# Optimization experiments

Hardware: AMD Instinct MI355X
Metric: run time of the kernel (lower is better)

Reference implementation:

```python
import jax, jax.numpy as jnp
import numpy as np

D = 256      # word_embd_size
V = 32000    # vocab_size_w
B, T, J = 32, 512, 128


def _gru_dir(x, wih, whh, bih, bhh):
    # x: (B, T, D); torch GRU cell convention
    def step(h, xt):
        gi = xt @ wih.T + bih            # (B, 3D)
        gh = h @ whh.T + bhh
        i_r, i_z, i_n = jnp.split(gi, 3, axis=-1)
        h_r, h_z, h_n = jnp.split(gh, 3, axis=-1)
        r = jax.nn.sigmoid(i_r + h_r)
        z = jax.nn.sigmoid(i_z + h_z)
        n = jnp.tanh(i_n + r * h_n)
        h_new = (1.0 - z) * n + z * h
        return h_new, h_new
    h0 = jnp.zeros((x.shape[0], D), dtype=x.dtype)
    _, ys = jax.lax.scan(step, h0, jnp.swapaxes(x, 0, 1))
    return jnp.swapaxes(ys, 0, 1)         # (B, T, D)


def _bigru(x, wih_f, whh_f, bih_f, bhh_f, wih_b, whh_b, bih_b, bhh_b):
    fwd = _gru_dir(x, wih_f, whh_f, bih_f, bhh_f)
    bwd = jnp.flip(_gru_dir(jnp.flip(x, 1), wih_b, whh_b, bih_b, bhh_b), 1)
    return jnp.concatenate([fwd, bwd], axis=-1)   # (B, T, 2D)


def _cmnt_sim(ctx, cmnt_e, action, w2):
    # Fused form of: S = W2_ha(cat(ctx_ex * cmnt_ex, action_ex)) over (B,T,J,2D+1)
    # S[b,t,j] = sum_d ctx[b,t,d]*cmnt[b,j,d]*w2[d] + action[b,t]*w2[2D]
    S = jnp.einsum('btd,bjd->btj', ctx * w2[:2 * D], cmnt_e)
    S = S + action.astype(ctx.dtype)[:, :, None] * w2[2 * D]
    b = jax.nn.softmax(jnp.max(S, axis=2), axis=-1)   # (B, T)
    return jnp.einsum('bt,btj->bj', b, S)             # (B, J)


def setup_inputs() -> dict:
    key = jax.random.key(0)
    ks = jax.random.split(key, 20)
    s = 1.0 / np.sqrt(D)
    u = lambda k, shape: jax.random.uniform(k, shape, minval=-s, maxval=s, dtype=jnp.float32)
    return {
        'cmnt': jax.random.randint(ks[0], (B, J), 0, V),
        'src_token': jax.random.randint(ks[1], (B, T), 0, V),
        'tgt_token': jax.random.randint(ks[2], (B, T), 0, V),
        'src_action': jax.random.randint(ks[3], (B, T), 0, 2),
        'tgt_action': jax.random.randint(ks[4], (B, T), 0, 2),
        'emb': jax.random.normal(ks[5], (V, D), dtype=jnp.float32) * 0.02,
        'wih_f': u(ks[6], (3 * D, D)), 'whh_f': u(ks[7], (3 * D, D)),
        'bih_f': u(ks[8], (3 * D,)),  'bhh_f': u(ks[9], (3 * D,)),
        'wih_b': u(ks[10], (3 * D, D)), 'whh_b': u(ks[11], (3 * D, D)),
        'bih_b': u(ks[12], (3 * D,)),  'bhh_b': u(ks[13], (3 * D,)),
        'w2': u(ks[14], (2 * D + 1,)),
        'rank_w': u(ks[15], (2 * J, 1)),
        'rank_b': u(ks[16], (1,)),
    }


def reference(cmnt, src_token, tgt_token, src_action, tgt_action, emb,
              wih_f, whh_f, bih_f, bhh_f, wih_b, whh_b, bih_b, bhh_b,
              w2, rank_w, rank_b):
    gru = lambda x: _bigru(x, wih_f, whh_f, bih_f, bhh_f, wih_b, whh_b, bih_b, bhh_b)
    e_src = gru(emb[src_token])    # (B, T, 2D)
    e_tgt = gru(emb[tgt_token])    # (B, T, 2D)
    e_cmnt = gru(emb[cmnt])        # (B, J, 2D)
    S_src = _cmnt_sim(e_src, e_cmnt, src_action, w2)
    S_tgt = _cmnt_sim(e_tgt, e_cmnt, tgt_action, w2)
    S_diff = jnp.concatenate([S_src, S_tgt], axis=1)   # (B, 2J)
    result = S_diff @ rank_w + rank_b                   # (B, 1)
    return result, S_diff
```

## Files before the change

kernel.cpp:

```cpp
#include <hip/hip_runtime.h>
#include <math.h>

#define DD   256
#define TTT  512
#define JJJ  128
#define BBB  32
#define NC   1536
#define ROWS_ALL 36864

typedef _Float16 v2h __attribute__((ext_vector_type(2)));
typedef _Float16 v4h __attribute__((ext_vector_type(4)));
typedef _Float16 v8h __attribute__((ext_vector_type(8)));
typedef short short8 __attribute__((ext_vector_type(8)));
typedef float f32x4 __attribute__((ext_vector_type(4)));

#if __has_builtin(__builtin_amdgcn_fdot2)
#define FDOT2(a, b, c) __builtin_amdgcn_fdot2((a), (b), (c), false)
#else
#define FDOT2(a, b, c) ((float)(a)[0] * (float)(b)[0] + ((float)(a)[1] * (float)(b)[1] + (c)))
#endif

__device__ __forceinline__ short f2bf(float f) {
    unsigned u = __float_as_uint(f);
    unsigned r = (u + 0x7FFFu + ((u >> 16) & 1u)) >> 16;
    return (short)r;
}

__global__ __launch_bounds__(256) void prep_kernel(
    const int* __restrict__ cmnt, const int* __restrict__ src_tok, const int* __restrict__ tgt_tok,
    const float* __restrict__ wih_f, const float* __restrict__ wih_b,
    const float* __restrict__ whh_f, const float* __restrict__ whh_b,
    const float* __restrict__ bih_f, const float* __restrict__ bih_b,
    const float* __restrict__ bhh_f, const float* __restrict__ bhh_b,
    const float* __restrict__ w2,
    int* __restrict__ tok_all, float* __restrict__ whhT,
    float* __restrict__ bihc, float* __restrict__ bhhc, short* __restrict__ Bt,
    _Float16* __restrict__ w2h)
{
    const int idx = blockIdx.x * blockDim.x + threadIdx.x;
    const int stride = gridDim.x * blockDim.x;
    for (int i = idx; i < ROWS_ALL; i += stride)
        tok_all[i] = (i < 16384) ? src_tok[i] : (i < 32768) ? tgt_tok[i - 16384] : cmnt[i - 32768];
    for (int i = idx; i < 256 * NC; i += stride) {
        const int k = i / NC, c = i % NC;
        whhT[i] = (c < 768) ? whh_f[(size_t)c * 256 + k] : whh_b[(size_t)(c - 768) * 256 + k];
    }
    for (int i = idx; i < 393216; i += stride)
        Bt[i] = f2bf(i < 196608 ? wih_f[i] : wih_b[i - 196608]);
    for (int i = idx; i < NC; i += stride) {
        bihc[i] = (i < 768) ? bih_f[i] : bih_b[i - 768];
        bhhc[i] = (i < 768) ? bhh_f[i] : bhh_b[i - 768];
    }
    for (int i = idx; i < 512; i += stride)
        w2h[i] = (_Float16)w2[i];
}

__global__ __launch_bounds__(256) void gatherA_kernel(
    const int* __restrict__ tok, int row_start, int nrows,
    const float* __restrict__ emb, short* __restrict__ A)
{
    const int idx = blockIdx.x * blockDim.x + threadIdx.x;
    const int stride = gridDim.x * blockDim.x;
    const int ngroups = nrows * 64;
    for (int g = idx; g < ngroups; g += stride) {
        const int i = g >> 6;
        const int kq = (g & 63) << 2;
        const float4 v = *(const float4*)(emb + (size_t)tok[row_start + i] * 256 + kq);
        short4 s;
        s.x = f2bf(v.x); s.y = f2bf(v.y); s.z = f2bf(v.z); s.w = f2bf(v.w);
        *(short4*)(A + (size_t)i * 256 + kq) = s;
    }
}

#define LP 40
__global__ __launch_bounds__(256) void gi_mfma(
    const short* __restrict__ A, const short* __restrict__ Bt,
    const float* __restrict__ bihc, _Float16* __restrict__ gi)
{
    __shared__ __align__(16) short As[128 * LP];
    __shared__ __align__(16) short Bs[128 * LP];
    const int tid = threadIdx.x;
    const int wave = tid >> 6, lane = tid & 63;
    const int quad = lane >> 4, l16 = lane & 15;
    const int m0 = blockIdx.x * 128, n0 = blockIdx.y * 128;
    const int wm = (wave & 1) * 64, wn = (wave >> 1) * 64;

    const int sr = tid >> 2;
    const int sk = (tid & 3) * 8;
    const short* ga0 = A  + (size_t)(m0 + sr) * 256 + sk;
    const short* ga1 = A  + (size_t)(m0 + sr + 64) * 256 + sk;
    const short* gb0 = Bt + (size_t)(n0 + sr) * 256 + sk;
    const short* gb1 = Bt + (size_t)(n0 + sr + 64) * 256 + sk;

    f32x4 acc[4][4];
    #pragma unroll
    for (int i = 0; i < 4; ++i)
        #pragma unroll
        for (int j = 0; j < 4; ++j) acc[i][j] = (f32x4){0.f, 0.f, 0.f, 0.f};

    for (int k0 = 0; k0 < 256; k0 += 32) {
        const short8 a0 = *(const short8*)(ga0 + k0);
        const short8 a1 = *(const short8*)(ga1 + k0);
        const short8 b0 = *(const short8*)(gb0 + k0);
        const short8 b1 = *(const short8*)(gb1 + k0);
        __syncthreads();
        *(short8*)&As[sr * LP + sk] = a0;
        *(short8*)&As[(sr + 64) * LP + sk] = a1;
        *(short8*)&Bs[sr * LP + sk] = b0;
        *(short8*)&Bs[(sr + 64) * LP + sk] = b1;
        __syncthreads();
        short8 af[4], bf[4];
        #pragma unroll
        for (int i = 0; i < 4; ++i)
            af[i] = *(const short8*)&As[(wm + i * 16 + l16) * LP + quad * 8];
        #pragma unroll
        for (int j = 0; j < 4; ++j)
            bf[j] = *(const short8*)&Bs[(wn + j * 16 + l16) * LP + quad * 8];
        #pragma unroll
        for (int i = 0; i < 4; ++i)
            #pragma unroll
            for (int j = 0; j < 4; ++j)
                acc[i][j] = __builtin_amdgcn_mfma_f32_16x16x32_bf16(af[i], bf[j], acc[i][j], 0, 0, 0);
    }

    #pragma unroll
    for (int j = 0; j < 4; ++j) {
        const int col = n0 + wn + j * 16 + l16;
        const float bias = bihc[col];
        #pragma unroll
        for (int i = 0; i < 4; ++i) {
            const int r0 = m0 + wm + i * 16 + quad * 4;
            #pragma unroll
            for (int reg = 0; reg < 4; ++reg)
                gi[(size_t)(r0 + reg) * NC + col] = (_Float16)(acc[i][j][reg] + bias);
        }
    }
}

__global__ __launch_bounds__(512, 2) void gru_kernel(
    const _Float16* __restrict__ gi0, const _Float16* __restrict__ gi1, const _Float16* __restrict__ gi2,
    const float* __restrict__ whhT, const float* __restrict__ bhhc,
    _Float16* __restrict__ e_src, _Float16* __restrict__ e_tgt, _Float16* __restrict__ e_cmnt,
    int chain_base)
{
    const int chain = chain_base + (int)(blockIdx.x >> 5);
    const int b = (int)(blockIdx.x & 31);
    const int seq = chain >> 1, dir = chain & 1;
    const int Tlen = (seq == 2) ? JJJ : TTT;
    const _Float16* gi = (seq == 0) ? gi0 : (seq == 1) ? gi1 : gi2;
    _Float16* e = (seq == 0) ? e_src : (seq == 1) ? e_tgt : e_cmnt;

    const int tid = threadIdx.x;
    const int j = tid & 255;
    const int q = tid >> 8;
    const int cb = dir * 768;

    __shared__ __align__(16) v2h h2s[128];
    __shared__ float parts[3][256];

    v2h wr2[64], wz2[64], wn2[64];
    {
        const float* wb = whhT + (size_t)(q * 128) * NC + cb + j;
        #pragma unroll
        for (int p = 0; p < 64; ++p) {
            v2h a, bzv, c;
            a[0]   = (_Float16)wb[0];        a[1]   = (_Float16)wb[NC];
            bzv[0] = (_Float16)wb[256];      bzv[1] = (_Float16)wb[NC + 256];
            c[0]   = (_Float16)wb[512];      c[1]   = (_Float16)wb[NC + 512];
            wr2[p] = a; wz2[p] = bzv; wn2[p] = c;
            wb += 2 * NC;
        }
    }
    const float br  = bhhc[cb + j];
    const float bzb = bhhc[cb + 256 + j];
    const float bnb = bhhc[cb + 512 + j];

    float hprev = 0.f;
    if (q == 0 && (j & 1) == 0) {
        v2h z0; z0[0] = (_Float16)0.f; z0[1] = (_Float16)0.f;
        h2s[j >> 1] = z0;
    }
    __syncthreads();

    const int t0i = dir ? (Tlen - 1) : 0;
    const long tstep = dir ? -1 : 1;
    const _Float16* girow = gi + (size_t)(b * Tlen + t0i) * NC + cb;
    _Float16* eptr = e + (size_t)(b * Tlen + t0i) * 512 + (dir << 8) + j;
    const long gstep = tstep * NC;
    const long estep = tstep * 512;

    _Float16* pptr = eptr;
    float pval = 0.f;

    for (int s = 0; s < Tlen; ++s) {
        float gr_ = 0.f, gz_ = 0.f, gn_ = 0.f;
        if (q == 0) {
            if (s > 0) *pptr = (_Float16)pval;
            gr_ = (float)girow[j];
            gz_ = (float)girow[256 + j];
            gn_ = (float)girow[512 + j];
        }

        float ar = 0.f, az = 0.f, an = 0.f;
        const v2h* hbase = &h2s[q * 64];
        #pragma unroll
        for (int c = 0; c < 16; ++c) {
            union { float4 f; v2h h[4]; } U;
            U.f = *(const float4*)&hbase[c * 4];
            #pragma unroll
            for (int p = 0; p < 4; ++p) {
                ar = FDOT2(wr2[c * 4 + p], U.h[p], ar);
                az = FDOT2(wz2[c * 4 + p], U.h[p], az);
                an = FDOT2(wn2[c * 4 + p], U.h[p], an);
            }
        }
        if (q == 1) { parts[0][j] = ar; parts[1][j] = az; parts[2][j] = an; }
        __syncthreads();

        if (q == 0) {
            const float sr = ar + parts[0][j] + br;
            const float sz = az + parts[1][j] + bzb;
            const float sn = an + parts[2][j] + bnb;
            const float r = 1.f / (1.f + __expf(-(gr_ + sr)));
            const float z = 1.f / (1.f + __expf(-(gz_ + sz)));
            const float xa = gn_ + r * sn;
            const float texp = __expf(2.f * xa);
            const float n = 1.f - 2.f / (texp + 1.f);
            const float hnew = (1.f - z) * n + z * hprev;
            hprev = hnew;
            pptr = eptr; pval = hnew;
            const float hnb = __shfl_xor(hnew, 1);
            if ((j & 1) == 0) {
                v2h hv; hv[0] = (_Float16)hnew; hv[1] = (_Float16)hnb;
                h2s[j >> 1] = hv;
            }
        }
        girow += gstep;
        eptr += estep;
        __syncthreads();
    }
    if (q == 0) *pptr = (_Float16)pval;
}

__global__ __launch_bounds__(256) void sim_mfma(
    const _Float16* __restrict__ e_src, const _Float16* __restrict__ e_tgt,
    const _Float16* __restrict__ e_cmnt, const _Float16* __restrict__ w2h,
    const float* __restrict__ w2,
    const int* __restrict__ src_action, const int* __restrict__ tgt_action,
    float* __restrict__ S, float* __restrict__ rowmaxP)
{
    const int sb = (int)blockIdx.z;
    const int seq = sb >> 5, b = sb & 31;
    const int t0 = blockIdx.x * 128;
    const _Float16* ctx = ((seq == 0) ? e_src : e_tgt) + (size_t)b * 512 * 512;
    const _Float16* ec = e_cmnt + (size_t)b * 128 * 512;
    const int* act = (seq == 0) ? src_action : tgt_action;

    __shared__ __align__(16) _Float16 As[128 * LP];
    __shared__ __align__(16) _Float16 Bs[128 * LP];
    const int tid = threadIdx.x;
    const int wave = tid >> 6, lane = tid & 63;
    const int quad = lane >> 4, l16 = lane & 15;
    const int wm = (wave & 1) * 64, wn = (wave >> 1) * 64;
    const int sr = tid >> 2;
    const int sk = (tid & 3) * 8;

    const _Float16* ga0 = ctx + (size_t)(t0 + sr) * 512 + sk;
    const _Float16* ga1 = ctx + (size_t)(t0 + sr + 64) * 512 + sk;
    const _Float16* gb0 = ec + (size_t)sr * 512 + sk;
    const _Float16* gb1 = ec + (size_t)(sr + 64) * 512 + sk;

    f32x4 acc[4][4];
    #pragma unroll
    for (int i = 0; i < 4; ++i)
        #pragma unroll
        for (int j = 0; j < 4; ++j) acc[i][j] = (f32x4){0.f, 0.f, 0.f, 0.f};

    for (int k0 = 0; k0 < 512; k0 += 32) {
        v8h a0 = *(const v8h*)(ga0 + k0);
        v8h a1 = *(const v8h*)(ga1 + k0);
        const v8h b0 = *(const v8h*)(gb0 + k0);
        const v8h b1 = *(const v8h*)(gb1 + k0);
        const v8h w8 = *(const v8h*)(w2h + k0 + sk);
        a0 = a0 * w8;
        a1 = a1 * w8;
        __syncthreads();
        *(v8h*)&As[sr * LP + sk] = a0;
        *(v8h*)&As[(sr + 64) * LP + sk] = a1;
        *(v8h*)&Bs[sr * LP + sk] = b0;
        *(v8h*)&Bs[(sr + 64) * LP + sk] = b1;
        __syncthreads();
        v8h af[4], bf[4];
        #pragma unroll
        for (int i = 0; i < 4; ++i)
            af[i] = *(const v8h*)&As[(wm + i * 16 + l16) * LP + quad * 8];
        #pragma unroll
        for (int j = 0; j < 4; ++j)
            bf[j] = *(const v8h*)&Bs[(wn + j * 16 + l16) * LP + quad * 8];
        #pragma unroll
        for (int i = 0; i < 4; ++i)
            #pragma unroll
            for (int j = 0; j < 4; ++j)
                acc[i][j] = __builtin_amdgcn_mfma_f32_16x16x32_f16(af[i], bf[j], acc[i][j], 0, 0, 0);
    }

    const float w2a = w2[512];
    #pragma unroll
    for (int i = 0; i < 4; ++i) {
        #pragma unroll
        for (int reg = 0; reg < 4; ++reg) {
            const int t = t0 + wm + i * 16 + quad * 4 + reg;
            const float aterm = (float)act[b * 512 + t] * w2a;
            float m = -1e30f;
            #pragma unroll
            for (int j = 0; j < 4; ++j) {
                const float v = acc[i][j][reg] + aterm;
                S[((size_t)(sb * 512 + t)) * 128 + wn + j * 16 + l16] = v;
                m = fmaxf(m, v);
            }
            m = fmaxf(m, __shfl_xor(m, 1));
            m = fmaxf(m, __shfl_xor(m, 2));
            m = fmaxf(m, __shfl_xor(m, 4));
            m = fmaxf(m, __shfl_xor(m, 8));
            if (l16 == 0)
                rowmaxP[(size_t)(wave >> 1) * 32768 + sb * 512 + t] = m;
        }
    }
}

__global__ __launch_bounds__(256) void softmax_kernel(const float* __restrict__ rowmaxP, float* __restrict__ bw)
{
    const int base = blockIdx.x * 512;
    const int tid = threadIdx.x;
    __shared__ float red[256];
    const float v0 = fmaxf(rowmaxP[base + tid], rowmaxP[32768 + base + tid]);
    const float v1 = fmaxf(rowmaxP[base + 256 + tid], rowmaxP[32768 + base + 256 + tid]);
    red[tid] = fmaxf(v0, v1);
    __syncthreads();
    for (int off = 128; off > 0; off >>= 1) {
        if (tid < off) red[tid] = fmaxf(red[tid], red[tid + off]);
        __syncthreads();
    }
    const float M = red[0];
    __syncthreads();
    const float e0 = __expf(v0 - M), e1 = __expf(v1 - M);
    red[tid] = e0 + e1;
    __syncthreads();
    for (int off = 128; off > 0; off >>= 1) {
        if (tid < off) red[tid] += red[tid + off];
        __syncthreads();
    }
    const float inv = 1.f / red[0];
    bw[base + tid] = e0 * inv;
    bw[base + 256 + tid] = e1 * inv;
}

__global__ __launch_bounds__(256) void weighted_kernel(
    const float* __restrict__ S, const float* __restrict__ bw, float* __restrict__ outSP)
{
    const int sb = blockIdx.x;
    const int ch = blockIdx.y;
    const int tid = threadIdx.x;
    const int j = tid & 127, half = tid >> 7;
    const float* Sb = S + (size_t)sb * 512 * 128;
    const float* w = bw + sb * 512;
    const int tb = ch * 64 + half * 32;
    float acc = 0.f;
    for (int t = tb; t < tb + 32; ++t)
        acc = fmaf(w[t], Sb[(size_t)t * 128 + j], acc);
    __shared__ float red[256];
    red[tid] = acc;
    __syncthreads();
    if (half == 0) outSP[(size_t)ch * 8192 + sb * 128 + j] = red[j] + red[128 + j];
}

__global__ __launch_bounds__(256) void final_kernel(
    const float* __restrict__ outSP, const float* __restrict__ rank_w,
    const float* __restrict__ rank_b, float* __restrict__ out)
{
    __shared__ float sArr[8192];
    const int tid = threadIdx.x;
    for (int q = tid; q < 8192; q += 256) {
        float s = 0.f;
        #pragma unroll
        for (int c = 0; c < 8; ++c) s += outSP[(size_t)c * 8192 + q];
        sArr[q] = s;
    }
    __syncthreads();
    for (int q = tid; q < 8192; q += 256) {
        const int b = q >> 8, c = q & 255;
        out[32 + q] = (c < 128) ? sArr[b * 128 + c] : sArr[4096 + b * 128 + (c - 128)];
    }
    if (tid < 32) {
        float acc = rank_b[0];
        for (int c = 0; c < 128; ++c) acc = fmaf(sArr[tid * 128 + c], rank_w[c], acc);
        for (int c = 0; c < 128; ++c) acc = fmaf(sArr[4096 + tid * 128 + c], rank_w[128 + c], acc);
        out[tid] = acc;
    }
}

extern "C" void kernel_launch(void* const* d_in, const int* in_sizes, int n_in,
                              void* d_out, int out_size, void* d_ws, size_t ws_size,
                              hipStream_t stream)
{
    const int* cmnt       = (const int*)d_in[0];
    const int* src_token  = (const int*)d_in[1];
    const int* tgt_token  = (const int*)d_in[2];
    const int* src_action = (const int*)d_in[3];
    const int* tgt_action = (const int*)d_in[4];
    const float* emb    = (const float*)d_in[5];
    const float* wih_f  = (const float*)d_in[6];
    const float* whh_f  = (const float*)d_in[7];
    const float* bih_f  = (const float*)d_in[8];
    const float* bhh_f  = (const float*)d_in[9];
    const float* wih_b  = (const float*)d_in[10];
    const float* whh_b  = (const float*)d_in[11];
    const float* bih_b  = (const float*)d_in[12];
    const float* bhh_b  = (const float*)d_in[13];
    const float* w2     = (const float*)d_in[14];
    const float* rank_w = (const float*)d_in[15];
    const float* rank_b = (const float*)d_in[16];
    float* out = (float*)d_out;

    float* ws = (float*)d_ws;
    size_t off = 0;
    int*   tok_all = (int*)(ws + off); off += 36864;
    short* Bt_bf16 = (short*)(ws + off); off += 196608;
    float* whhT   = ws + off; off += 393216;
    float* bihc   = ws + off; off += 1536;
    float* bhhc   = ws + off; off += 1536;
    _Float16* w2h = (_Float16*)(ws + off); off += 256;
    float* rowmaxP = ws + off; off += 65536;
    float* bw     = ws + off; off += 32768;
    float* outSP  = ws + off; off += 65536;
    _Float16* e_src  = (_Float16*)(ws + off); off += 4194304;
    _Float16* e_tgt  = (_Float16*)(ws + off); off += 4194304;
    _Float16* e_cmnt = (_Float16*)(ws + off); off += 1048576;
    float* S      = ws + off; off += 4194304;
    _Float16* gih = (_Float16*)(ws + off);
    const size_t avail = ws_size / 4 - off;
    const bool planP = avail >= 28311552ULL;

    hipLaunchKernelGGL(prep_kernel, dim3(512), dim3(256), 0, stream,
        cmnt, src_token, tgt_token, wih_f, wih_b, whh_f, whh_b,
        bih_f, bih_b, bhh_f, bhh_b, w2, tok_all, whhT, bihc, bhhc, Bt_bf16, w2h);

    if (planP) {
        short* A = (short*)e_src;
        hipLaunchKernelGGL(gatherA_kernel, dim3(4096), dim3(256), 0, stream,
            tok_all, 0, 36864, emb, A);
        hipLaunchKernelGGL(gi_mfma, dim3(288, 12), dim3(256), 0, stream,
            A, Bt_bf16, bihc, gih);
        hipLaunchKernelGGL(gru_kernel, dim3(192), dim3(512), 0, stream,
            gih, gih + (size_t)16384 * NC, gih + (size_t)32768 * NC,
            whhT, bhhc, e_src, e_tgt, e_cmnt, 0);
    } else {
        short* A = (short*)S;
        const int starts[3] = {0, 16384, 32768};
        const int nrows[3]  = {16384, 16384, 4096};
        for (int sq = 0; sq < 3; ++sq) {
            hipLaunchKernelGGL(gatherA_kernel, dim3(4096), dim3(256), 0, stream,
                tok_all, starts[sq], nrows[sq], emb, A);
            hipLaunchKernelGGL(gi_mfma, dim3(nrows[sq] / 128, 12), dim3(256), 0, stream,
                A, Bt_bf16, bihc, gih);
            hipLaunchKernelGGL(gru_kernel, dim3(64), dim3(512), 0, stream,
                gih, gih, gih, whhT, bhhc, e_src, e_tgt, e_cmnt, 2 * sq);
        }
    }

    hipLaunchKernelGGL(sim_mfma, dim3(4, 1, 64), dim3(256), 0, stream,
        e_src, e_tgt, e_cmnt, w2h, w2, src_action, tgt_action, S, rowmaxP);
    hipLaunchKernelGGL(softmax_kernel, dim3(64), dim3(256), 0, stream, rowmaxP, bw);
    hipLaunchKernelGGL(weighted_kernel, dim3(64, 8), dim3(256), 0, stream, S, bw, outSP);
    hipLaunchKernelGGL(final_kernel, dim3(1), dim3(256), 0, stream, outSP, rank_w, rank_b, out);
}
```

Baseline: 844.8 us.

## Batch GRU recurrence over 16 sequences per block using MFMA

The GRU recurrence kernel is restructured so that each block handles 16 batch rows of one chain and runs the h·Whh^T product with f16 MFMA instructions, keeping Whh fragments in registers. Previously each block ran a single batch element with scalar fdot2 and a split-K reduction through shared memory. The input-gate GEMM now writes its output in a swizzled layout matched to the MFMA lane mapping and folds the r/z hidden biases into it. The low-memory fallback plan is removed. The grid shrinks from 192 blocks to 12, so only 12 CUs work through the long sequential chain. Each step now does larger MFMA work per block, which risks poor overall occupancy.

```diff
diff --git a/kernel.cpp b/kernel.cpp
--- a/kernel.cpp
+++ b/kernel.cpp
@@ -13,12 +13,6 @@
 typedef _Float16 v8h __attribute__((ext_vector_type(8)));
 typedef short short8 __attribute__((ext_vector_type(8)));
 typedef float f32x4 __attribute__((ext_vector_type(4)));
-
-#if __has_builtin(__builtin_amdgcn_fdot2)
-#define FDOT2(a, b, c) __builtin_amdgcn_fdot2((a), (b), (c), false)
-#else
-#define FDOT2(a, b, c) ((float)(a)[0] * (float)(b)[0] + ((float)(a)[1] * (float)(b)[1] + (c)))
-#endif
 
 __device__ __forceinline__ short f2bf(float f) {
     unsigned u = __float_as_uint(f);
@@ -33,7 +27,7 @@
     const float* __restrict__ bih_f, const float* __restrict__ bih_b,
     const float* __restrict__ bhh_f, const float* __restrict__ bhh_b,
     const float* __restrict__ w2,
-    int* __restrict__ tok_all, float* __restrict__ whhT,
+    int* __restrict__ tok_all, _Float16* __restrict__ wh16,
     float* __restrict__ bihc, float* __restrict__ bhhc, short* __restrict__ Bt,
     _Float16* __restrict__ w2h)
 {
@@ -41,10 +35,8 @@
     const int stride = gridDim.x * blockDim.x;
     for (int i = idx; i < ROWS_ALL; i += stride)
         tok_all[i] = (i < 16384) ? src_tok[i] : (i < 32768) ? tgt_tok[i - 16384] : cmnt[i - 32768];
-    for (int i = idx; i < 256 * NC; i += stride) {
-        const int k = i / NC, c = i % NC;
-        whhT[i] = (c < 768) ? whh_f[(size_t)c * 256 + k] : whh_b[(size_t)(c - 768) * 256 + k];
-    }
+    for (int i = idx; i < 393216; i += stride)
+        wh16[i] = (_Float16)(i < 196608 ? whh_f[i] : whh_b[i - 196608]);
     for (int i = idx; i < 393216; i += stride)
         Bt[i] = f2bf(i < 196608 ? wih_f[i] : wih_b[i - 196608]);
     for (int i = idx; i < NC; i += stride) {
@@ -56,7 +48,7 @@
 }
 
 __global__ __launch_bounds__(256) void gatherA_kernel(
-    const int* __restrict__ tok, int row_start, int nrows,
+    const int* __restrict__ tok, int nrows,
     const float* __restrict__ emb, short* __restrict__ A)
 {
     const int idx = blockIdx.x * blockDim.x + threadIdx.x;
@@ -65,7 +57,7 @@
     for (int g = idx; g < ngroups; g += stride) {
         const int i = g >> 6;
         const int kq = (g & 63) << 2;
-        const float4 v = *(const float4*)(emb + (size_t)tok[row_start + i] * 256 + kq);
+        const float4 v = *(const float4*)(emb + (size_t)tok[i] * 256 + kq);
         short4 s;
         s.x = f2bf(v.x); s.y = f2bf(v.y); s.z = f2bf(v.z); s.w = f2bf(v.w);
         *(short4*)(A + (size_t)i * 256 + kq) = s;
@@ -75,7 +67,8 @@
 #define LP 40
 __global__ __launch_bounds__(256) void gi_mfma(
     const short* __restrict__ A, const short* __restrict__ Bt,
-    const float* __restrict__ bihc, _Float16* __restrict__ gi)
+    const float* __restrict__ bihc, const float* __restrict__ bhhc,
+    _Float16* __restrict__ gi_swz)
 {
     __shared__ __align__(16) short As[128 * LP];
     __shared__ __align__(16) short Bs[128 * LP];
@@ -123,123 +116,151 @@
                 acc[i][j] = __builtin_amdgcn_mfma_f32_16x16x32_bf16(af[i], bf[j], acc[i][j], 0, 0, 0);
     }
 
-    #pragma unroll
-    for (int j = 0; j < 4; ++j) {
-        const int col = n0 + wn + j * 16 + l16;
-        const float bias = bihc[col];
-        #pragma unroll
-        for (int i = 0; i < 4; ++i) {
-            const int r0 = m0 + wm + i * 16 + quad * 4;
-            #pragma unroll
-            for (int reg = 0; reg < 4; ++reg)
-                gi[(size_t)(r0 + reg) * NC + col] = (_Float16)(acc[i][j][reg] + bias);
+    const int seq = (m0 >= 32768) ? 2 : (m0 >= 16384 ? 1 : 0);
+    const int rowbase = seq * 16384;
+    const int logT = (seq == 2) ? 7 : 9;
+    const int tmask = (1 << logT) - 1;
+    const int seqTbase = (seq == 0) ? 0 : (seq == 1) ? 512 : 1024;
+
+    int colpart[4];
+    float bias[4];
+    #pragma unroll
+    for (int jj = 0; jj < 4; ++jj) {
+        const int c = n0 + wn + jj * 16 + l16;
+        const int dir = (c >= 768) ? 1 : 0;
+        const int cg = c - dir * 768;
+        const int g = cg >> 8;
+        const int jloc = cg & 255;
+        colpart[jj] = dir * 24576 + (jloc >> 5) * 1536 + (jloc & 15) * 24
+                      + g * 8 + ((jloc >> 4) & 1) * 4;
+        bias[jj] = bihc[c] + ((g < 2) ? bhhc[c] : 0.f);
+    }
+    #pragma unroll
+    for (int i = 0; i < 4; ++i) {
+        #pragma unroll
+        for (int reg = 0; reg < 4; ++reg) {
+            const int rowloc = m0 + wm + i * 16 + quad * 4 + reg - rowbase;
+            const int b = rowloc >> logT;
+            const int t = rowloc & tmask;
+            const size_t rowpart = (size_t)(seqTbase + t) * 49152
+                                   + (b >> 4) * 12288 + ((b >> 2) & 3) * 384 + (b & 3);
+            #pragma unroll
+            for (int jj = 0; jj < 4; ++jj)
+                gi_swz[rowpart + colpart[jj]] = (_Float16)(acc[i][jj][reg] + bias[jj]);
         }
     }
 }
 
 __global__ __launch_bounds__(512, 2) void gru_kernel(
-    const _Float16* __restrict__ gi0, const _Float16* __restrict__ gi1, const _Float16* __restrict__ gi2,
-    const float* __restrict__ whhT, const float* __restrict__ bhhc,
-    _Float16* __restrict__ e_src, _Float16* __restrict__ e_tgt, _Float16* __restrict__ e_cmnt,
-    int chain_base)
-{
-    const int chain = chain_base + (int)(blockIdx.x >> 5);
-    const int b = (int)(blockIdx.x & 31);
+    const _Float16* __restrict__ gi_swz, const _Float16* __restrict__ wh16,
+    const float* __restrict__ bhhc,
+    _Float16* __restrict__ e_src, _Float16* __restrict__ e_tgt, _Float16* __restrict__ e_cmnt)
+{
+    const int chain = (int)(blockIdx.x >> 1);
+    const int bhalf = (int)(blockIdx.x & 1);
     const int seq = chain >> 1, dir = chain & 1;
     const int Tlen = (seq == 2) ? JJJ : TTT;
-    const _Float16* gi = (seq == 0) ? gi0 : (seq == 1) ? gi1 : gi2;
+    const int seqTbase = (seq == 0) ? 0 : (seq == 1) ? 512 : 1024;
     _Float16* e = (seq == 0) ? e_src : (seq == 1) ? e_tgt : e_cmnt;
-
-    const int tid = threadIdx.x;
-    const int j = tid & 255;
-    const int q = tid >> 8;
     const int cb = dir * 768;
 
-    __shared__ __align__(16) v2h h2s[128];
-    __shared__ float parts[3][256];
-
-    v2h wr2[64], wz2[64], wn2[64];
-    {
-        const float* wb = whhT + (size_t)(q * 128) * NC + cb + j;
-        #pragma unroll
-        for (int p = 0; p < 64; ++p) {
-            v2h a, bzv, c;
-            a[0]   = (_Float16)wb[0];        a[1]   = (_Float16)wb[NC];
-            bzv[0] = (_Float16)wb[256];      bzv[1] = (_Float16)wb[NC + 256];
-            c[0]   = (_Float16)wb[512];      c[1]   = (_Float16)wb[NC + 512];
-            wr2[p] = a; wz2[p] = bzv; wn2[p] = c;
-            wb += 2 * NC;
-        }
-    }
-    const float br  = bhhc[cb + j];
-    const float bzb = bhhc[cb + 256 + j];
-    const float bnb = bhhc[cb + 512 + j];
-
-    float hprev = 0.f;
-    if (q == 0 && (j & 1) == 0) {
-        v2h z0; z0[0] = (_Float16)0.f; z0[1] = (_Float16)0.f;
-        h2s[j >> 1] = z0;
-    }
-    __syncthreads();
-
-    const int t0i = dir ? (Tlen - 1) : 0;
-    const long tstep = dir ? -1 : 1;
-    const _Float16* girow = gi + (size_t)(b * Tlen + t0i) * NC + cb;
-    _Float16* eptr = e + (size_t)(b * Tlen + t0i) * 512 + (dir << 8) + j;
-    const long gstep = tstep * NC;
-    const long estep = tstep * 512;
-
-    _Float16* pptr = eptr;
-    float pval = 0.f;
+    const int tid = threadIdx.x;
+    const int w = tid >> 6, lane = tid & 63;
+    const int quad = lane >> 4, l16 = lane & 15;
+    const int j0 = w * 32;
+
+    __shared__ __align__(16) _Float16 hbuf[2][16 * 264];
+
+    v8h Wf[3][2][8];
+    #pragma unroll
+    for (int g = 0; g < 3; ++g)
+        #pragma unroll
+        for (int u = 0; u < 2; ++u) {
+            const _Float16* wrow = wh16 + (size_t)(cb + g * 256 + j0 + u * 16 + l16) * 256 + quad * 8;
+            #pragma unroll
+            for (int ks = 0; ks < 8; ++ks)
+                Wf[g][u][ks] = *(const v8h*)(wrow + ks * 32);
+        }
+
+    float bhn[2];
+    #pragma unroll
+    for (int u = 0; u < 2; ++u) bhn[u] = bhhc[cb + 512 + j0 + u * 16 + l16];
+
+    float hp[2][4];
+    #pragma unroll
+    for (int u = 0; u < 2; ++u)
+        #pragma unroll
+        for (int reg = 0; reg < 4; ++reg) hp[u][reg] = 0.f;
+
+    for (int i = tid; i < 16 * 264; i += 512) hbuf[0][i] = (_Float16)0.f;
+    __syncthreads();
+
+    const int t0 = dir ? (Tlen - 1) : 0;
+    const _Float16* gp = gi_swz
+        + ((size_t)(seqTbase + t0) * 2048 + (size_t)(dir * 1024 + bhalf * 512 + tid)) * 24;
+    const long gistep = (dir ? -1L : 1L) * 49152;
+
+    _Float16* ecur = e + ((size_t)(bhalf * 16 + quad * 4) * Tlen + t0) * 512 + dir * 256 + j0 + l16;
+    const long estep = (dir ? -1L : 1L) * 512;
+    const long eregstride = (long)Tlen * 512;
+    _Float16* epend = ecur;
 
     for (int s = 0; s < Tlen; ++s) {
-        float gr_ = 0.f, gz_ = 0.f, gn_ = 0.f;
-        if (q == 0) {
-            if (s > 0) *pptr = (_Float16)pval;
-            gr_ = (float)girow[j];
-            gz_ = (float)girow[256 + j];
-            gn_ = (float)girow[512 + j];
-        }
-
-        float ar = 0.f, az = 0.f, an = 0.f;
-        const v2h* hbase = &h2s[q * 64];
-        #pragma unroll
-        for (int c = 0; c < 16; ++c) {
-            union { float4 f; v2h h[4]; } U;
-            U.f = *(const float4*)&hbase[c * 4];
-            #pragma unroll
-            for (int p = 0; p < 4; ++p) {
-                ar = FDOT2(wr2[c * 4 + p], U.h[p], ar);
-                az = FDOT2(wz2[c * 4 + p], U.h[p], az);
-                an = FDOT2(wn2[c * 4 + p], U.h[p], an);
+        const v8h g0 = *(const v8h*)(gp);
+        const v8h g1 = *(const v8h*)(gp + 8);
+        const v8h g2 = *(const v8h*)(gp + 16);
+        if (s > 0) {
+            #pragma unroll
+            for (int u = 0; u < 2; ++u)
+                #pragma unroll
+                for (int reg = 0; reg < 4; ++reg)
+                    epend[(long)reg * eregstride + u * 16] = (_Float16)hp[u][reg];
+        }
+
+        f32x4 acc[3][2];
+        #pragma unroll
+        for (int g = 0; g < 3; ++g)
+            #pragma unroll
+            for (int u = 0; u < 2; ++u) acc[g][u] = (f32x4){0.f, 0.f, 0.f, 0.f};
+
+        const _Float16* hb = &hbuf[s & 1][l16 * 264 + quad * 8];
+        #pragma unroll
+        for (int ks = 0; ks < 8; ++ks) {
+            const v8h Af = *(const v8h*)(hb + ks * 32);
+            #pragma unroll
+            for (int g = 0; g < 3; ++g)
+                #pragma unroll
+                for (int u = 0; u < 2; ++u)
+                    acc[g][u] = __builtin_amdgcn_mfma_f32_16x16x32_f16(Af, Wf[g][u][ks], acc[g][u], 0, 0, 0);
+        }
+
+        _Float16* hw = &hbuf[(s + 1) & 1][(quad * 4) * 264 + j0 + l16];
+        #pragma unroll
+        for (int u = 0; u < 2; ++u) {
+            #pragma unroll
+            for (int reg = 0; reg < 4; ++reg) {
+                const float gr = acc[0][u][reg] + (float)g0[u * 4 + reg];
+                const float gz = acc[1][u][reg] + (float)g1[u * 4 + reg];
+                const float r = 1.f / (1.f + __expf(-gr));
+                const float z = 1.f / (1.f + __expf(-gz));
+                const float x = (float)g2[u * 4 + reg] + r * (acc[2][u][reg] + bhn[u]);
+                const float ex = __expf(2.f * x);
+                const float n = 1.f - 2.f / (ex + 1.f);
+                const float hnew = (1.f - z) * n + z * hp[u][reg];
+                hp[u][reg] = hnew;
+                hw[reg * 264 + u * 16] = (_Float16)hnew;
             }
         }
-        if (q == 1) { parts[0][j] = ar; parts[1][j] = az; parts[2][j] = an; }
-        __syncthreads();
-
-        if (q == 0) {
-            const float sr = ar + parts[0][j] + br;
-            const float sz = az + parts[1][j] + bzb;
-            const float sn = an + parts[2][j] + bnb;
-            const float r = 1.f / (1.f + __expf(-(gr_ + sr)));
-            const float z = 1.f / (1.f + __expf(-(gz_ + sz)));
-            const float xa = gn_ + r * sn;
-            const float texp = __expf(2.f * xa);
-            const float n = 1.f - 2.f / (texp + 1.f);
-            const float hnew = (1.f - z) * n + z * hprev;
-            hprev = hnew;
-            pptr = eptr; pval = hnew;
-            const float hnb = __shfl_xor(hnew, 1);
-            if ((j & 1) == 0) {
-                v2h hv; hv[0] = (_Float16)hnew; hv[1] = (_Float16)hnb;
-                h2s[j >> 1] = hv;
-            }
-        }
-        girow += gstep;
-        eptr += estep;
-        __syncthreads();
-    }
-    if (q == 0) *pptr = (_Float16)pval;
+        epend = ecur;
+        ecur += estep;
+        gp += gistep;
+        __syncthreads();
+    }
+    #pragma unroll
+    for (int u = 0; u < 2; ++u)
+        #pragma unroll
+        for (int reg = 0; reg < 4; ++reg)
+            epend[(long)reg * eregstride + u * 16] = (_Float16)hp[u][reg];
 }
 
 __global__ __launch_bounds__(256) void sim_mfma(
@@ -426,7 +447,7 @@
     size_t off = 0;
     int*   tok_all = (int*)(ws + off); off += 36864;
     short* Bt_bf16 = (short*)(ws + off); off += 196608;
-    float* whhT   = ws + off; off += 393216;
+    _Float16* wh16 = (_Float16*)(ws + off); off += 196608;
     float* bihc   = ws + off; off += 1536;
     float* bhhc   = ws + off; off += 1536;
     _Float16* w2h = (_Float16*)(ws + off); off += 256;
@@ -437,36 +458,19 @@
     _Float16* e_tgt  = (_Float16*)(ws + off); off += 4194304;
     _Float16* e_cmnt = (_Float16*)(ws + off); off += 1048576;
     float* S      = ws + off; off += 4194304;
-    _Float16* gih = (_Float16*)(ws + off);
-    const size_t avail = ws_size / 4 - off;
-    const bool planP = avail >= 28311552ULL;
+    _Float16* gi_swz = (_Float16*)(ws + off);
 
     hipLaunchKernelGGL(prep_kernel, dim3(512), dim3(256), 0, stream,
         cmnt, src_token, tgt_token, wih_f, wih_b, whh_f, whh_b,
-        bih_f, bih_b, bhh_f, bhh_b, w2, tok_all, whhT, bihc, bhhc, Bt_bf16, w2h);
-
-    if (planP) {
-        short* A = (short*)e_src;
-        hipLaunchKernelGGL(gatherA_kernel, dim3(4096), dim3(256), 0, stream,
-            tok_all, 0, 36864, emb, A);
-        hipLaunchKernelGGL(gi_mfma, dim3(288, 12), dim3(256), 0, stream,
-            A, Bt_bf16, bihc, gih);
-        hipLaunchKernelGGL(gru_kernel, dim3(192), dim3(512), 0, stream,
-            gih, gih + (size_t)16384 * NC, gih + (size_t)32768 * NC,
-            whhT, bhhc, e_src, e_tgt, e_cmnt, 0);
-    } else {
-        short* A = (short*)S;
-        const int starts[3] = {0, 16384, 32768};
-        const int nrows[3]  = {16384, 16384, 4096};
-        for (int sq = 0; sq < 3; ++sq) {
-            hipLaunchKernelGGL(gatherA_kernel, dim3(4096), dim3(256), 0, stream,
-                tok_all, starts[sq], nrows[sq], emb, A);
-            hipLaunchKernelGGL(gi_mfma, dim3(nrows[sq] / 128, 12), dim3(256), 0, stream,
-                A, Bt_bf16, bihc, gih);
-            hipLaunchKernelGGL(gru_kernel, dim3(64), dim3(512), 0, stream,
-                gih, gih, gih, whhT, bhhc, e_src, e_tgt, e_cmnt, 2 * sq);
-        }
-    }
+        bih_f, bih_b, bhh_f, bhh_b, w2, tok_all, wh16, bihc, bhhc, Bt_bf16, w2h);
+
+    short* A = (short*)e_src;
+    hipLaunchKernelGGL(gatherA_kernel, dim3(4096), dim3(256), 0, stream,
+        tok_all, 36864, emb, A);
+    hipLaunchKernelGGL(gi_mfma, dim3(288, 12), dim3(256), 0, stream,
+        A, Bt_bf16, bihc, bhhc, gi_swz);
+    hipLaunchKernelGGL(gru_kernel, dim3(12), dim3(512), 0, stream,
+        gi_swz, wh16, bhhc, e_src, e_tgt, e_cmnt);
 
     hipLaunchKernelGGL(sim_mfma, dim3(4, 1, 64), dim3(256), 0, stream,
         e_src, e_tgt, e_cmnt, w2h, w2, src_action, tgt_action, S, rowmaxP);
```

Result: slower. 1.765 ms (+108.9%).
